# Kernel tuning notes

Measured on AMD Instinct MI355X. Metric: run time of the kernel, lower is better.

Reference implementation:

```python
import jax, jax.numpy as jnp
import numpy as np

N_NODES = 100000
N_EDGES = 1600000
F_IN = 256
F_OUT = 32


def setup_inputs() -> dict:
    key = jax.random.key(0)
    k1, k2, k3 = jax.random.split(key, 3)
    x = jax.random.normal(k1, (N_NODES, F_IN), dtype=jnp.float32)
    edge_index = jax.random.randint(k2, (2, N_EDGES), 0, N_NODES, dtype=jnp.int64)
    W = jax.random.normal(k3, (F_IN, F_OUT), dtype=jnp.float32) / np.sqrt(F_IN)
    b = jnp.zeros((F_OUT,), dtype=jnp.float32)
    return {"x": x, "edge_index": edge_index, "W": W, "b": b}


def reference(x, edge_index, W, b):
    # PyG GCNConv: add self-loops, symmetric normalization, linear, aggregate.
    N = x.shape[0]
    loop = jnp.arange(N, dtype=edge_index.dtype)
    src = jnp.concatenate([edge_index[0], loop])  # message sources
    dst = jnp.concatenate([edge_index[1], loop])  # aggregation targets

    deg = jax.ops.segment_sum(jnp.ones_like(dst, dtype=x.dtype), dst,
                              num_segments=N)
    deg_inv_sqrt = jnp.where(deg > 0, jax.lax.rsqrt(jnp.maximum(deg, 1.0)), 0.0)
    norm = deg_inv_sqrt[src] * deg_inv_sqrt[dst]  # [E+N]

    h = x @ W  # [N, F_OUT] transform first (as PyG does)
    msg = h[src] * norm[:, None]  # gather + scale
    out = jax.ops.segment_sum(msg, dst, num_segments=N) + b
    return out
```

## Files before the change

### kernel.cpp

```cpp
#include <hip/hip_runtime.h>

#define F_IN  256
#define F_OUT 32

#define NPB       512
#define NPB_SHIFT 9
#define NB2MAX    256
#define EPW       8192
#define BCAP      10240

typedef __attribute__((ext_vector_type(8))) short bf16x8;
typedef __attribute__((ext_vector_type(4))) float f32x4;

__device__ __forceinline__ short f2bf(float f) {
    unsigned u = __float_as_uint(f);
    u += 0x7FFF + ((u >> 16) & 1);
    return (short)(u >> 16);
}

__global__ __launch_bounds__(256) void k_zero(int* __restrict__ bcur,
                                              const int* __restrict__ ei,
                                              int* __restrict__ flag) {
    int i = blockIdx.x * 256 + threadIdx.x;
    if (i < NB2MAX) bcur[i] = i * BCAP;
    if (i == 0) {
        int o = 0;
        for (int k = 1; k < 64; k += 2) o |= ei[k];
        *flag = (o == 0) ? 1 : 0;
    }
}

__global__ __launch_bounds__(1024) void k_bucket(const int* __restrict__ ei,
                                                 const int* __restrict__ flag,
                                                 int* __restrict__ bcur,
                                                 int* __restrict__ ebuf,
                                                 int E, int N) {
    __shared__ int lhist[NB2MAX];
    __shared__ int lbase[NB2MAX];
    __shared__ int sP[EPW];
    __shared__ unsigned short sB[EPW];
    const int tid = threadIdx.x;
    if (tid < NB2MAX) lhist[tid] = 0;
    __syncthreads();
    const int m64 = *flag;
    const long long e0 = (long long)blockIdx.x * EPW;
    #pragma unroll
    for (int jj = 0; jj < EPW / 2048; ++jj) {
        int p = jj * 1024 + tid;
        long long e = e0 + 2 * (long long)p;
        int s0 = -1, d0 = -1, s1 = -1, d1 = -1;
        if (e + 1 < E) {
            if (m64) {
                int4 sv = ((const int4*)ei)[p + (e0 >> 1) * 0];
                sv = ((const int4*)(ei))[(size_t)(e >> 1)];
                int4 dv = ((const int4*)(ei + 2 * (size_t)E))[(size_t)(e >> 1)];
                s0 = sv.x; s1 = sv.z; d0 = dv.x; d1 = dv.z;
            } else {
                int2 sv = ((const int2*)(ei))[(size_t)(e >> 1)];
                int2 dv = ((const int2*)(ei + (size_t)E))[(size_t)(e >> 1)];
                s0 = sv.x; s1 = sv.y; d0 = dv.x; d1 = dv.y;
            }
        } else if (e < E) {
            if (m64) { s0 = ei[2 * (size_t)e]; d0 = ei[2 * ((size_t)E + e)]; }
            else     { s0 = ei[(size_t)e];     d0 = ei[(size_t)E + e]; }
        }
        unsigned short bb0 = 0xFFFF, bb1 = 0xFFFF;
        int pk0 = 0, pk1 = 0;
        if ((unsigned)d0 < (unsigned)N && (unsigned)s0 < (unsigned)N) {
            bb0 = (unsigned short)(d0 >> NPB_SHIFT);
            pk0 = s0 | ((d0 & (NPB - 1)) << 23);
            atomicAdd(&lhist[bb0], 1);
        }
        if ((unsigned)d1 < (unsigned)N && (unsigned)s1 < (unsigned)N) {
            bb1 = (unsigned short)(d1 >> NPB_SHIFT);
            pk1 = s1 | ((d1 & (NPB - 1)) << 23);
            atomicAdd(&lhist[bb1], 1);
        }
        sB[2 * p] = bb0;     sP[2 * p] = pk0;
        sB[2 * p + 1] = bb1; sP[2 * p + 1] = pk1;
    }
    __syncthreads();
    if (tid < NB2MAX) {
        int c = lhist[tid];
        lbase[tid] = c ? atomicAdd(&bcur[tid], c) : 0;
        lhist[tid] = 0;
    }
    __syncthreads();
    #pragma unroll 4
    for (int j = 0; j < EPW / 1024; ++j) {
        int idx = j * 1024 + tid;
        unsigned short bb = sB[idx];
        if (bb != 0xFFFF) {
            int slot = lbase[bb] + atomicAdd(&lhist[bb], 1);
            if (slot < (int)(bb + 1) * BCAP) ebuf[slot] = sP[idx];
        }
    }
}

__global__ __launch_bounds__(1024) void k_sort(int* __restrict__ ebuf,
                                               const int* __restrict__ bcur,
                                               float* __restrict__ dinv,
                                               int* __restrict__ offp, int N) {
    __shared__ int sedge[BCAP];
    __shared__ int lcnt[NPB];
    __shared__ int lofs[NPB];
    __shared__ int sc[NPB];
    const int tid = threadIdx.x;
    const int b = blockIdx.x;
    const int start = b * BCAP;
    const int m = min(max(bcur[b] - start, 0), BCAP);

    {
        const int4* src4 = (const int4*)(ebuf + start);
        int m4 = m >> 2;
        for (int i = tid; i < m4; i += 1024)
            ((int4*)sedge)[i] = src4[i];
        for (int i = (m4 << 2) + tid; i < m; i += 1024)
            sedge[i] = ebuf[start + i];
    }
    if (tid < NPB) lcnt[tid] = 0;
    __syncthreads();
    for (int i = tid; i < m; i += 1024)
        atomicAdd(&lcnt[((unsigned)sedge[i]) >> 23], 1);
    __syncthreads();
    int c0 = (tid < NPB) ? lcnt[tid] : 0;
    int val = c0;
    if (tid < NPB) sc[tid] = val;
    __syncthreads();
    #pragma unroll
    for (int d2 = 1; d2 < NPB; d2 <<= 1) {
        int t = (tid < NPB && tid >= d2) ? sc[tid - d2] : 0;
        __syncthreads();
        if (tid < NPB) { val += t; sc[tid] = val; }
        __syncthreads();
    }
    if (tid < NPB) {
        int excl = val - c0;
        lofs[tid] = excl;
        int n = (b << NPB_SHIFT) + tid;
        if (n < N) {
            dinv[n] = rsqrtf((float)c0 + 1.0f);
            offp[n] = (start + excl) | (min(c0, 1023) << 22);
        }
    }
    __syncthreads();
    for (int i = tid; i < m; i += 1024) {
        int pk = sedge[i];
        int l = ((unsigned)pk) >> 23;
        int slot = start + atomicAdd(&lofs[l], 1);
        ebuf[slot] = pk & 0x7FFFFF;
    }
}

#define WLDP 264
__global__ __launch_bounds__(256) void k_gemm(const float* __restrict__ x,
                                              const float* __restrict__ W,
                                              const float* __restrict__ dinv,
                                              _Float16* __restrict__ hs16, int N) {
    __shared__ __align__(16) short sWt[F_OUT * WLDP];
    const int tid = threadIdx.x;
    const int lane = tid & 63;
    const int wave = tid >> 6;
    const int row0 = blockIdx.x * 128 + wave * 32;

    for (int i = tid; i < F_IN * F_OUT; i += 256) {
        int f = i & 31, k = i >> 5;
        sWt[f * WLDP + k] = f2bf(W[i]);
    }
    __syncthreads();

    const int l15 = lane & 15;
    const int lg  = lane >> 4;
    int ra = row0 + l15;
    int rb = row0 + 16 + l15;
    int rac = min(ra, N - 1);
    int rbc = min(rb, N - 1);

    const float4* xa4 = (const float4*)(x + (size_t)rac * F_IN + lg * 8);
    const float4* xb4 = (const float4*)(x + (size_t)rbc * F_IN + lg * 8);
    const short* wb0 = sWt + l15 * WLDP + lg * 8;
    const short* wb1 = sWt + (16 + l15) * WLDP + lg * 8;

    f32x4 acc00 = {0.f, 0.f, 0.f, 0.f};
    f32x4 acc01 = {0.f, 0.f, 0.f, 0.f};
    f32x4 acc10 = {0.f, 0.f, 0.f, 0.f};
    f32x4 acc11 = {0.f, 0.f, 0.f, 0.f};

    float4 a0 = xa4[0], a1 = xa4[1];
    float4 b0 = xb4[0], b1 = xb4[1];

    #pragma unroll
    for (int kb = 0; kb < F_IN / 32; ++kb) {
        float4 na0, na1, nb0, nb1;
        if (kb < F_IN / 32 - 1) {
            na0 = xa4[(kb + 1) * 8];
            na1 = xa4[(kb + 1) * 8 + 1];
            nb0 = xb4[(kb + 1) * 8];
            nb1 = xb4[(kb + 1) * 8 + 1];
        }
        bf16x8 A0, A1;
        A0[0] = f2bf(a0.x); A0[1] = f2bf(a0.y); A0[2] = f2bf(a0.z); A0[3] = f2bf(a0.w);
        A0[4] = f2bf(a1.x); A0[5] = f2bf(a1.y); A0[6] = f2bf(a1.z); A0[7] = f2bf(a1.w);
        A1[0] = f2bf(b0.x); A1[1] = f2bf(b0.y); A1[2] = f2bf(b0.z); A1[3] = f2bf(b0.w);
        A1[4] = f2bf(b1.x); A1[5] = f2bf(b1.y); A1[6] = f2bf(b1.z); A1[7] = f2bf(b1.w);
        bf16x8 B0 = *(const bf16x8*)(wb0 + kb * 32);
        bf16x8 B1 = *(const bf16x8*)(wb1 + kb * 32);
        acc00 = __builtin_amdgcn_mfma_f32_16x16x32_bf16(A0, B0, acc00, 0, 0, 0);
        acc01 = __builtin_amdgcn_mfma_f32_16x16x32_bf16(A0, B1, acc01, 0, 0, 0);
        acc10 = __builtin_amdgcn_mfma_f32_16x16x32_bf16(A1, B0, acc10, 0, 0, 0);
        acc11 = __builtin_amdgcn_mfma_f32_16x16x32_bf16(A1, B1, acc11, 0, 0, 0);
        a0 = na0; a1 = na1; b0 = nb0; b1 = nb1;
    }

    #pragma unroll
    for (int r = 0; r < 4; ++r) {
        int row = row0 + lg * 4 + r;
        if (row < N) {
            float di = dinv[row];
            hs16[(size_t)row * F_OUT + l15]      = (_Float16)(acc00[r] * di);
            hs16[(size_t)row * F_OUT + 16 + l15] = (_Float16)(acc01[r] * di);
        }
        int row2 = row + 16;
        if (row2 < N) {
            float di2 = dinv[row2];
            hs16[(size_t)row2 * F_OUT + l15]      = (_Float16)(acc10[r] * di2);
            hs16[(size_t)row2 * F_OUT + 16 + l15] = (_Float16)(acc11[r] * di2);
        }
    }
}

__global__ __launch_bounds__(256) void k_agg(const _Float16* __restrict__ hs16,
                                             const int* __restrict__ adj,
                                             const int* __restrict__ offp,
                                             const float* __restrict__ dinv,
                                             const float* __restrict__ bias,
                                             float* __restrict__ out, int N) {
    const int tid = threadIdx.x;
    const int n = blockIdx.x * 64 + (tid >> 2);
    const int q = tid & 3;
    if (n >= N) return;

    const int po = offp[n];
    const int st = po & 0x3FFFFF;
    const int deg = ((unsigned)po) >> 22;

    const uint4* __restrict__ h4 = (const uint4*)hs16;
    union U { uint4 u; _Float16 h[8]; };

    float a[8], c[8];
    {
        U sv; sv.u = h4[(size_t)n * 4 + q];
        #pragma unroll
        for (int i = 0; i < 8; ++i) { a[i] = (float)sv.h[i]; c[i] = 0.f; }
    }

    int k = 0;
    if (deg >= 8) {
        int s[8];
        #pragma unroll
        for (int j = 0; j < 8; ++j) s[j] = adj[st + j];
        while (k + 16 <= deg) {
            U v0, v1, v2, v3, v4, v5, v6, v7;
            v0.u = h4[(size_t)s[0] * 4 + q];
            v1.u = h4[(size_t)s[1] * 4 + q];
            v2.u = h4[(size_t)s[2] * 4 + q];
            v3.u = h4[(size_t)s[3] * 4 + q];
            v4.u = h4[(size_t)s[4] * 4 + q];
            v5.u = h4[(size_t)s[5] * 4 + q];
            v6.u = h4[(size_t)s[6] * 4 + q];
            v7.u = h4[(size_t)s[7] * 4 + q];
            int ns[8];
            #pragma unroll
            for (int j = 0; j < 8; ++j) ns[j] = adj[st + k + 8 + j];
            #pragma unroll
            for (int i = 0; i < 8; ++i) {
                a[i] += ((float)v0.h[i] + (float)v1.h[i]) +
                        ((float)v2.h[i] + (float)v3.h[i]);
                c[i] += ((float)v4.h[i] + (float)v5.h[i]) +
                        ((float)v6.h[i] + (float)v7.h[i]);
            }
            #pragma unroll
            for (int j = 0; j < 8; ++j) s[j] = ns[j];
            k += 8;
        }
        {
            U v0, v1, v2, v3, v4, v5, v6, v7;
            v0.u = h4[(size_t)s[0] * 4 + q];
            v1.u = h4[(size_t)s[1] * 4 + q];
            v2.u = h4[(size_t)s[2] * 4 + q];
            v3.u = h4[(size_t)s[3] * 4 + q];
            v4.u = h4[(size_t)s[4] * 4 + q];
            v5.u = h4[(size_t)s[5] * 4 + q];
            v6.u = h4[(size_t)s[6] * 4 + q];
            v7.u = h4[(size_t)s[7] * 4 + q];
            #pragma unroll
            for (int i = 0; i < 8; ++i) {
                a[i] += ((float)v0.h[i] + (float)v1.h[i]) +
                        ((float)v2.h[i] + (float)v3.h[i]);
                c[i] += ((float)v4.h[i] + (float)v5.h[i]) +
                        ((float)v6.h[i] + (float)v7.h[i]);
            }
            k += 8;
        }
    }
    for (; k + 4 <= deg; k += 4) {
        int s0 = adj[st + k];
        int s1 = adj[st + k + 1];
        int s2 = adj[st + k + 2];
        int s3 = adj[st + k + 3];
        U v0, v1, v2, v3;
        v0.u = h4[(size_t)s0 * 4 + q];
        v1.u = h4[(size_t)s1 * 4 + q];
        v2.u = h4[(size_t)s2 * 4 + q];
        v3.u = h4[(size_t)s3 * 4 + q];
        #pragma unroll
        for (int i = 0; i < 8; ++i)
            a[i] += ((float)v0.h[i] + (float)v1.h[i]) +
                    ((float)v2.h[i] + (float)v3.h[i]);
    }
    for (; k < deg; ++k) {
        int s0 = adj[st + k];
        U v0; v0.u = h4[(size_t)s0 * 4 + q];
        #pragma unroll
        for (int i = 0; i < 8; ++i) a[i] += (float)v0.h[i];
    }

    const float di = dinv[n];
    const float4 bv0 = ((const float4*)bias)[q * 2];
    const float4 bv1 = ((const float4*)bias)[q * 2 + 1];
    float4 o0, o1;
    o0.x = bv0.x + di * (a[0] + c[0]); o0.y = bv0.y + di * (a[1] + c[1]);
    o0.z = bv0.z + di * (a[2] + c[2]); o0.w = bv0.w + di * (a[3] + c[3]);
    o1.x = bv1.x + di * (a[4] + c[4]); o1.y = bv1.y + di * (a[5] + c[5]);
    o1.z = bv1.z + di * (a[6] + c[6]); o1.w = bv1.w + di * (a[7] + c[7]);
    float4* op = (float4*)(out + (size_t)n * F_OUT);
    op[q * 2]     = o0;
    op[q * 2 + 1] = o1;
}

extern "C" void kernel_launch(void* const* d_in, const int* in_sizes, int n_in,
                              void* d_out, int out_size, void* d_ws, size_t ws_size,
                              hipStream_t stream) {
    const float* x  = (const float*)d_in[0];
    const int*   ei = (const int*)d_in[1];
    const float* W  = (const float*)d_in[2];
    const float* b  = (const float*)d_in[3];
    float* out = (float*)d_out;

    const int N = in_sizes[0] / F_IN;
    const int E = in_sizes[1] / 2;

    _Float16* hs16 = (_Float16*)d_ws;
    int*   ebuf = (int*)(hs16 + (size_t)N * F_OUT);
    float* dinv = (float*)(ebuf + (size_t)NB2MAX * BCAP);
    int*   offp = (int*)(dinv + N);
    int*   bcur = offp + N;
    int*   flag = bcur + NB2MAX;

    const int NB  = (N + NPB - 1) >> NPB_SHIFT;
    const int NBW = (int)(((long long)E + EPW - 1) / EPW);

    k_zero  <<<1, 256, 0, stream>>>(bcur, ei, flag);
    k_bucket<<<NBW, 1024, 0, stream>>>(ei, flag, bcur, ebuf, E, N);
    k_sort  <<<NB, 1024, 0, stream>>>(ebuf, bcur, dinv, offp, N);
    k_gemm  <<<(N + 127) / 128, 256, 0, stream>>>(x, W, dinv, hs16, N);
    k_agg   <<<(N * 4 + 255) / 256, 256, 0, stream>>>(hs16, ebuf, offp, dinv, b, out, N);
}
```

Measured before the change: 227.9 us.

## Fuse per-bucket sort into aggregation and count degrees with global atomics

```diff
diff --git a/kernel.cpp b/kernel.cpp
--- a/kernel.cpp
+++ b/kernel.cpp
@@ -18,10 +18,12 @@
     return (short)(u >> 16);
 }
 
-__global__ __launch_bounds__(256) void k_zero(int* __restrict__ bcur,
+__global__ __launch_bounds__(256) void k_zero(int* __restrict__ cnt,
+                                              int* __restrict__ bcur,
                                               const int* __restrict__ ei,
-                                              int* __restrict__ flag) {
+                                              int* __restrict__ flag, int N) {
     int i = blockIdx.x * 256 + threadIdx.x;
+    if (i < N) cnt[i] = 0;
     if (i < NB2MAX) bcur[i] = i * BCAP;
     if (i == 0) {
         int o = 0;
@@ -34,6 +36,7 @@
                                                  const int* __restrict__ flag,
                                                  int* __restrict__ bcur,
                                                  int* __restrict__ ebuf,
+                                                 int* __restrict__ cnt,
                                                  int E, int N) {
     __shared__ int lhist[NB2MAX];
     __shared__ int lbase[NB2MAX];
@@ -51,8 +54,7 @@
         int s0 = -1, d0 = -1, s1 = -1, d1 = -1;
         if (e + 1 < E) {
             if (m64) {
-                int4 sv = ((const int4*)ei)[p + (e0 >> 1) * 0];
-                sv = ((const int4*)(ei))[(size_t)(e >> 1)];
+                int4 sv = ((const int4*)(ei))[(size_t)(e >> 1)];
                 int4 dv = ((const int4*)(ei + 2 * (size_t)E))[(size_t)(e >> 1)];
                 s0 = sv.x; s1 = sv.z; d0 = dv.x; d1 = dv.z;
             } else {
@@ -70,11 +72,13 @@
             bb0 = (unsigned short)(d0 >> NPB_SHIFT);
             pk0 = s0 | ((d0 & (NPB - 1)) << 23);
             atomicAdd(&lhist[bb0], 1);
+            atomicAdd(&cnt[d0], 1);
         }
         if ((unsigned)d1 < (unsigned)N && (unsigned)s1 < (unsigned)N) {
             bb1 = (unsigned short)(d1 >> NPB_SHIFT);
             pk1 = s1 | ((d1 & (NPB - 1)) << 23);
             atomicAdd(&lhist[bb1], 1);
+            atomicAdd(&cnt[d1], 1);
         }
         sB[2 * p] = bb0;     sP[2 * p] = pk0;
         sB[2 * p + 1] = bb1; sP[2 * p + 1] = pk1;
@@ -97,65 +101,10 @@
     }
 }
 
-__global__ __launch_bounds__(1024) void k_sort(int* __restrict__ ebuf,
-                                               const int* __restrict__ bcur,
-                                               float* __restrict__ dinv,
-                                               int* __restrict__ offp, int N) {
-    __shared__ int sedge[BCAP];
-    __shared__ int lcnt[NPB];
-    __shared__ int lofs[NPB];
-    __shared__ int sc[NPB];
-    const int tid = threadIdx.x;
-    const int b = blockIdx.x;
-    const int start = b * BCAP;
-    const int m = min(max(bcur[b] - start, 0), BCAP);
-
-    {
-        const int4* src4 = (const int4*)(ebuf + start);
-        int m4 = m >> 2;
-        for (int i = tid; i < m4; i += 1024)
-            ((int4*)sedge)[i] = src4[i];
-        for (int i = (m4 << 2) + tid; i < m; i += 1024)
-            sedge[i] = ebuf[start + i];
-    }
-    if (tid < NPB) lcnt[tid] = 0;
-    __syncthreads();
-    for (int i = tid; i < m; i += 1024)
-        atomicAdd(&lcnt[((unsigned)sedge[i]) >> 23], 1);
-    __syncthreads();
-    int c0 = (tid < NPB) ? lcnt[tid] : 0;
-    int val = c0;
-    if (tid < NPB) sc[tid] = val;
-    __syncthreads();
-    #pragma unroll
-    for (int d2 = 1; d2 < NPB; d2 <<= 1) {
-        int t = (tid < NPB && tid >= d2) ? sc[tid - d2] : 0;
-        __syncthreads();
-        if (tid < NPB) { val += t; sc[tid] = val; }
-        __syncthreads();
-    }
-    if (tid < NPB) {
-        int excl = val - c0;
-        lofs[tid] = excl;
-        int n = (b << NPB_SHIFT) + tid;
-        if (n < N) {
-            dinv[n] = rsqrtf((float)c0 + 1.0f);
-            offp[n] = (start + excl) | (min(c0, 1023) << 22);
-        }
-    }
-    __syncthreads();
-    for (int i = tid; i < m; i += 1024) {
-        int pk = sedge[i];
-        int l = ((unsigned)pk) >> 23;
-        int slot = start + atomicAdd(&lofs[l], 1);
-        ebuf[slot] = pk & 0x7FFFFF;
-    }
-}
-
 #define WLDP 264
 __global__ __launch_bounds__(256) void k_gemm(const float* __restrict__ x,
                                               const float* __restrict__ W,
-                                              const float* __restrict__ dinv,
+                                              const int* __restrict__ cnt,
                                               _Float16* __restrict__ hs16, int N) {
     __shared__ __align__(16) short sWt[F_OUT * WLDP];
     const int tid = threadIdx.x;
@@ -216,126 +165,162 @@
     for (int r = 0; r < 4; ++r) {
         int row = row0 + lg * 4 + r;
         if (row < N) {
-            float di = dinv[row];
+            float di = rsqrtf((float)cnt[row] + 1.0f);
             hs16[(size_t)row * F_OUT + l15]      = (_Float16)(acc00[r] * di);
             hs16[(size_t)row * F_OUT + 16 + l15] = (_Float16)(acc01[r] * di);
         }
         int row2 = row + 16;
         if (row2 < N) {
-            float di2 = dinv[row2];
+            float di2 = rsqrtf((float)cnt[row2] + 1.0f);
             hs16[(size_t)row2 * F_OUT + l15]      = (_Float16)(acc10[r] * di2);
             hs16[(size_t)row2 * F_OUT + 16 + l15] = (_Float16)(acc11[r] * di2);
         }
     }
 }
 
-__global__ __launch_bounds__(256) void k_agg(const _Float16* __restrict__ hs16,
-                                             const int* __restrict__ adj,
-                                             const int* __restrict__ offp,
-                                             const float* __restrict__ dinv,
-                                             const float* __restrict__ bias,
-                                             float* __restrict__ out, int N) {
+__global__ __launch_bounds__(1024) void k_sortagg(const int* __restrict__ ebuf,
+                                                  const int* __restrict__ bcur,
+                                                  const _Float16* __restrict__ hs16,
+                                                  const float* __restrict__ bias,
+                                                  float* __restrict__ out, int N) {
+    __shared__ int sorted[BCAP];
+    __shared__ int lcnt[NPB];
+    __shared__ int lofs[NPB];
+    __shared__ int sc[NPB];
     const int tid = threadIdx.x;
-    const int n = blockIdx.x * 64 + (tid >> 2);
-    const int q = tid & 3;
-    if (n >= N) return;
-
-    const int po = offp[n];
-    const int st = po & 0x3FFFFF;
-    const int deg = ((unsigned)po) >> 22;
+    const int b = blockIdx.x;
+    const int start = b * BCAP;
+    const int m = min(max(bcur[b] - start, 0), BCAP);
+
+    if (tid < NPB) lcnt[tid] = 0;
+    __syncthreads();
+
+    const int4* e4 = (const int4*)(ebuf + start);
+    const int m4 = m >> 2;
+    for (int i = tid; i < m4; i += 1024) {
+        int4 v = e4[i];
+        atomicAdd(&lcnt[((unsigned)v.x) >> 23], 1);
+        atomicAdd(&lcnt[((unsigned)v.y) >> 23], 1);
+        atomicAdd(&lcnt[((unsigned)v.z) >> 23], 1);
+        atomicAdd(&lcnt[((unsigned)v.w) >> 23], 1);
+    }
+    for (int i = (m4 << 2) + tid; i < m; i += 1024)
+        atomicAdd(&lcnt[((unsigned)ebuf[start + i]) >> 23], 1);
+    __syncthreads();
+
+    int c0 = (tid < NPB) ? lcnt[tid] : 0;
+    int val = c0;
+    if (tid < NPB) sc[tid] = val;
+    __syncthreads();
+    #pragma unroll
+    for (int d2 = 1; d2 < NPB; d2 <<= 1) {
+        int t = (tid < NPB && tid >= d2) ? sc[tid - d2] : 0;
+        __syncthreads();
+        if (tid < NPB) { val += t; sc[tid] = val; }
+        __syncthreads();
+    }
+    if (tid < NPB) lofs[tid] = val - c0;
+    __syncthreads();
+
+    for (int i = tid; i < m4; i += 1024) {
+        int4 v = e4[i];
+        int l0 = ((unsigned)v.x) >> 23;
+        sorted[atomicAdd(&lofs[l0], 1)] = v.x & 0x7FFFFF;
+        int l1 = ((unsigned)v.y) >> 23;
+        sorted[atomicAdd(&lofs[l1], 1)] = v.y & 0x7FFFFF;
+        int l2 = ((unsigned)v.z) >> 23;
+        sorted[atomicAdd(&lofs[l2], 1)] = v.z & 0x7FFFFF;
+        int l3 = ((unsigned)v.w) >> 23;
+        sorted[atomicAdd(&lofs[l3], 1)] = v.w & 0x7FFFFF;
+    }
+    for (int i = (m4 << 2) + tid; i < m; i += 1024) {
+        int pk = ebuf[start + i];
+        int l = ((unsigned)pk) >> 23;
+        sorted[atomicAdd(&lofs[l], 1)] = pk & 0x7FFFFF;
+    }
+    __syncthreads();
 
     const uint4* __restrict__ h4 = (const uint4*)hs16;
     union U { uint4 u; _Float16 h[8]; };
-
-    float a[8], c[8];
-    {
-        U sv; sv.u = h4[(size_t)n * 4 + q];
-        #pragma unroll
-        for (int i = 0; i < 8; ++i) { a[i] = (float)sv.h[i]; c[i] = 0.f; }
-    }
-
-    int k = 0;
-    if (deg >= 8) {
-        int s[8];
-        #pragma unroll
-        for (int j = 0; j < 8; ++j) s[j] = adj[st + j];
-        while (k + 16 <= deg) {
-            U v0, v1, v2, v3, v4, v5, v6, v7;
-            v0.u = h4[(size_t)s[0] * 4 + q];
-            v1.u = h4[(size_t)s[1] * 4 + q];
-            v2.u = h4[(size_t)s[2] * 4 + q];
-            v3.u = h4[(size_t)s[3] * 4 + q];
-            v4.u = h4[(size_t)s[4] * 4 + q];
-            v5.u = h4[(size_t)s[5] * 4 + q];
-            v6.u = h4[(size_t)s[6] * 4 + q];
-            v7.u = h4[(size_t)s[7] * 4 + q];
-            int ns[8];
-            #pragma unroll
-            for (int j = 0; j < 8; ++j) ns[j] = adj[st + k + 8 + j];
-            #pragma unroll
-            for (int i = 0; i < 8; ++i) {
-                a[i] += ((float)v0.h[i] + (float)v1.h[i]) +
-                        ((float)v2.h[i] + (float)v3.h[i]);
-                c[i] += ((float)v4.h[i] + (float)v5.h[i]) +
-                        ((float)v6.h[i] + (float)v7.h[i]);
-            }
-            #pragma unroll
-            for (int j = 0; j < 8; ++j) s[j] = ns[j];
-            k += 8;
-        }
-        {
-            U v0, v1, v2, v3, v4, v5, v6, v7;
-            v0.u = h4[(size_t)s[0] * 4 + q];
-            v1.u = h4[(size_t)s[1] * 4 + q];
-            v2.u = h4[(size_t)s[2] * 4 + q];
-            v3.u = h4[(size_t)s[3] * 4 + q];
-            v4.u = h4[(size_t)s[4] * 4 + q];
-            v5.u = h4[(size_t)s[5] * 4 + q];
-            v6.u = h4[(size_t)s[6] * 4 + q];
-            v7.u = h4[(size_t)s[7] * 4 + q];
-            #pragma unroll
-            for (int i = 0; i < 8; ++i) {
-                a[i] += ((float)v0.h[i] + (float)v1.h[i]) +
-                        ((float)v2.h[i] + (float)v3.h[i]);
-                c[i] += ((float)v4.h[i] + (float)v5.h[i]) +
-                        ((float)v6.h[i] + (float)v7.h[i]);
-            }
-            k += 8;
-        }
-    }
-    for (; k + 4 <= deg; k += 4) {
-        int s0 = adj[st + k];
-        int s1 = adj[st + k + 1];
-        int s2 = adj[st + k + 2];
-        int s3 = adj[st + k + 3];
-        U v0, v1, v2, v3;
-        v0.u = h4[(size_t)s0 * 4 + q];
-        v1.u = h4[(size_t)s1 * 4 + q];
-        v2.u = h4[(size_t)s2 * 4 + q];
-        v3.u = h4[(size_t)s3 * 4 + q];
-        #pragma unroll
-        for (int i = 0; i < 8; ++i)
-            a[i] += ((float)v0.h[i] + (float)v1.h[i]) +
-                    ((float)v2.h[i] + (float)v3.h[i]);
-    }
-    for (; k < deg; ++k) {
-        int s0 = adj[st + k];
-        U v0; v0.u = h4[(size_t)s0 * 4 + q];
-        #pragma unroll
-        for (int i = 0; i < 8; ++i) a[i] += (float)v0.h[i];
-    }
-
-    const float di = dinv[n];
-    const float4 bv0 = ((const float4*)bias)[q * 2];
-    const float4 bv1 = ((const float4*)bias)[q * 2 + 1];
-    float4 o0, o1;
-    o0.x = bv0.x + di * (a[0] + c[0]); o0.y = bv0.y + di * (a[1] + c[1]);
-    o0.z = bv0.z + di * (a[2] + c[2]); o0.w = bv0.w + di * (a[3] + c[3]);
-    o1.x = bv1.x + di * (a[4] + c[4]); o1.y = bv1.y + di * (a[5] + c[5]);
-    o1.z = bv1.z + di * (a[6] + c[6]); o1.w = bv1.w + di * (a[7] + c[7]);
-    float4* op = (float4*)(out + (size_t)n * F_OUT);
-    op[q * 2]     = o0;
-    op[q * 2 + 1] = o1;
+    const int q = tid & 3;
+
+    #pragma unroll
+    for (int r = 0; r < 2; ++r) {
+        const int ln = r * 256 + (tid >> 2);
+        const int n = (b << NPB_SHIFT) + ln;
+        if (n < N) {
+            const int deg = lcnt[ln];
+            const int st = lofs[ln] - deg;
+
+            float a[8], c[8];
+            {
+                U sv; sv.u = h4[(size_t)n * 4 + q];
+                #pragma unroll
+                for (int i = 0; i < 8; ++i) { a[i] = (float)sv.h[i]; c[i] = 0.f; }
+            }
+
+            int k = 0;
+            for (; k + 8 <= deg; k += 8) {
+                int s0 = sorted[st + k];
+                int s1 = sorted[st + k + 1];
+                int s2 = sorted[st + k + 2];
+                int s3 = sorted[st + k + 3];
+                int s4 = sorted[st + k + 4];
+                int s5 = sorted[st + k + 5];
+                int s6 = sorted[st + k + 6];
+                int s7 = sorted[st + k + 7];
+                U v0, v1, v2, v3, v4, v5, v6, v7;
+                v0.u = h4[(size_t)s0 * 4 + q];
+                v1.u = h4[(size_t)s1 * 4 + q];
+                v2.u = h4[(size_t)s2 * 4 + q];
+                v3.u = h4[(size_t)s3 * 4 + q];
+                v4.u = h4[(size_t)s4 * 4 + q];
+                v5.u = h4[(size_t)s5 * 4 + q];
+                v6.u = h4[(size_t)s6 * 4 + q];
+                v7.u = h4[(size_t)s7 * 4 + q];
+                #pragma unroll
+                for (int i = 0; i < 8; ++i) {
+                    a[i] += ((float)v0.h[i] + (float)v1.h[i]) +
+                            ((float)v2.h[i] + (float)v3.h[i]);
+                    c[i] += ((float)v4.h[i] + (float)v5.h[i]) +
+                            ((float)v6.h[i] + (float)v7.h[i]);
+                }
+            }
+            for (; k + 4 <= deg; k += 4) {
+                int s0 = sorted[st + k];
+                int s1 = sorted[st + k + 1];
+                int s2 = sorted[st + k + 2];
+                int s3 = sorted[st + k + 3];
+                U v0, v1, v2, v3;
+                v0.u = h4[(size_t)s0 * 4 + q];
+                v1.u = h4[(size_t)s1 * 4 + q];
+                v2.u = h4[(size_t)s2 * 4 + q];
+                v3.u = h4[(size_t)s3 * 4 + q];
+                #pragma unroll
+                for (int i = 0; i < 8; ++i)
+                    a[i] += ((float)v0.h[i] + (float)v1.h[i]) +
+                            ((float)v2.h[i] + (float)v3.h[i]);
+            }
+            for (; k < deg; ++k) {
+                int s0 = sorted[st + k];
+                U v0; v0.u = h4[(size_t)s0 * 4 + q];
+                #pragma unroll
+                for (int i = 0; i < 8; ++i) a[i] += (float)v0.h[i];
+            }
+
+            const float di = rsqrtf((float)deg + 1.0f);
+            const float4 bv0 = ((const float4*)bias)[q * 2];
+            const float4 bv1 = ((const float4*)bias)[q * 2 + 1];
+            float4 o0, o1;
+            o0.x = bv0.x + di * (a[0] + c[0]); o0.y = bv0.y + di * (a[1] + c[1]);
+            o0.z = bv0.z + di * (a[2] + c[2]); o0.w = bv0.w + di * (a[3] + c[3]);
+            o1.x = bv1.x + di * (a[4] + c[4]); o1.y = bv1.y + di * (a[5] + c[5]);
+            o1.z = bv1.z + di * (a[6] + c[6]); o1.w = bv1.w + di * (a[7] + c[7]);
+            float4* op = (float4*)(out + (size_t)n * F_OUT);
+            op[q * 2]     = o0;
+            op[q * 2 + 1] = o1;
+        }
+    }
 }
 
 extern "C" void kernel_launch(void* const* d_in, const int* in_sizes, int n_in,
@@ -352,17 +337,15 @@
 
     _Float16* hs16 = (_Float16*)d_ws;
     int*   ebuf = (int*)(hs16 + (size_t)N * F_OUT);
-    float* dinv = (float*)(ebuf + (size_t)NB2MAX * BCAP);
-    int*   offp = (int*)(dinv + N);
-    int*   bcur = offp + N;
+    int*   cnt  = ebuf + (size_t)NB2MAX * BCAP;
+    int*   bcur = cnt + N;
     int*   flag = bcur + NB2MAX;
 
     const int NB  = (N + NPB - 1) >> NPB_SHIFT;
     const int NBW = (int)(((long long)E + EPW - 1) / EPW);
 
-    k_zero  <<<1, 256, 0, stream>>>(bcur, ei, flag);
-    k_bucket<<<NBW, 1024, 0, stream>>>(ei, flag, bcur, ebuf, E, N);
-    k_sort  <<<NB, 1024, 0, stream>>>(ebuf, bcur, dinv, offp, N);
-    k_gemm  <<<(N + 127) / 128, 256, 0, stream>>>(x, W, dinv, hs16, N);
-    k_agg   <<<(N * 4 + 255) / 256, 256, 0, stream>>>(hs16, ebuf, offp, dinv, b, out, N);
-}
+    k_zero   <<<(N + 255) / 256, 256, 0, stream>>>(cnt, bcur, ei, flag, N);
+    k_bucket <<<NBW, 1024, 0, stream>>>(ei, flag, bcur, ebuf, cnt, E, N);
+    k_gemm   <<<(N + 127) / 128, 256, 0, stream>>>(x, W, cnt, hs16, N);
+    k_sortagg<<<NB, 1024, 0, stream>>>(ebuf, bcur, hs16, b, out, N);
+}
```

After: 272.0 us. 1.19x slower.
